# Optimization experiments

Hardware: AMD Instinct MI355X
Metric: run time of the kernel (lower is better)

## Reference

```python
import jax, jax.numpy as jnp
import numpy as np

N_NODES = 100000
N_EDGES = 1600000
N_FEAT = 128
HIDDEN = 128
N_CLASSES = 64


def setup_inputs() -> dict:
    key = jax.random.key(0)
    ks = jax.random.split(key, 6)
    x = jax.random.normal(ks[0], (N_NODES, N_FEAT), dtype=jnp.float32)
    edge_index = jax.random.randint(ks[1], (2, N_EDGES), 0, N_NODES, dtype=jnp.int64)
    # Glorot-ish scaled weights
    W1_l = jax.random.normal(ks[2], (N_FEAT, HIDDEN), dtype=jnp.float32) / np.sqrt(N_FEAT)
    W1_r = jax.random.normal(ks[3], (N_FEAT, HIDDEN), dtype=jnp.float32) / np.sqrt(N_FEAT)
    W2_l = jax.random.normal(ks[4], (HIDDEN, N_CLASSES), dtype=jnp.float32) / np.sqrt(HIDDEN)
    W2_r = jax.random.normal(ks[5], (HIDDEN, N_CLASSES), dtype=jnp.float32) / np.sqrt(HIDDEN)
    b1 = jnp.zeros((HIDDEN,), dtype=jnp.float32)
    b2 = jnp.zeros((N_CLASSES,), dtype=jnp.float32)
    return {"x": x, "edge_index": edge_index, "W1_l": W1_l, "b1": b1,
            "W1_r": W1_r, "W2_l": W2_l, "b2": b2, "W2_r": W2_r}


def _sage_conv(h, src, dst, n_nodes, inv_deg, W_l, W_r, b):
    # mean aggregation of source-node features into destination nodes
    agg = jax.ops.segment_sum(h[src], dst, num_segments=n_nodes)  # [N, d]
    agg = agg * inv_deg[:, None]
    return agg @ W_l + h @ W_r + b


def reference(x, edge_index, W1_l, b1, W1_r, W2_l, b2, W2_r):
    src, dst = edge_index[0], edge_index[1]
    n = x.shape[0]
    deg = jax.ops.segment_sum(jnp.ones_like(dst, dtype=x.dtype), dst, num_segments=n)
    inv_deg = 1.0 / jnp.maximum(deg, 1.0)
    h = jax.nn.relu(_sage_conv(x, src, dst, n, inv_deg, W1_l, W1_r, b1))
    # dropout is identity in eval mode
    out = _sage_conv(h, src, dst, n, inv_deg, W2_l, W2_r, b2)
    return out
```

## Files before the change

### kernel.cpp

```cpp
#include <hip/hip_runtime.h>

#define N_NODES   100000
#define N_EDGES   1600000
#define BSHIFT    9
#define NB        196

typedef __attribute__((ext_vector_type(8))) short short8;
typedef __attribute__((ext_vector_type(4))) float f32x4;
typedef __attribute__((ext_vector_type(2))) float f32x2;

__device__ __forceinline__ unsigned short f2bf(float f) {
    unsigned u = __float_as_uint(f);
    u += 0x7FFF + ((u >> 16) & 1);
    return (unsigned short)(u >> 16);
}
__device__ __forceinline__ float bf2f(short s) {
    return __uint_as_float(((unsigned)(unsigned short)s) << 16);
}

__device__ __forceinline__ int load_src(const int* e, int is64, int i) {
    return is64 ? e[2 * i] : e[i];
}
__device__ __forceinline__ int load_dst(const int* e, int is64, int i) {
    return is64 ? e[2 * (N_EDGES + i)] : e[N_EDGES + i];
}

__device__ __forceinline__ int block_detect_is64(const int* e, int* s_nz) {
    if (threadIdx.x == 0) *s_nz = 0;
    __syncthreads();
    int v = 0;
    for (int i = threadIdx.x; i < 1024; i += 256) v |= e[2 * i + 1];
    if (v) atomicOr(s_nz, 1);
    __syncthreads();
    return (*s_nz == 0) ? 1 : 0;
}

__global__ __launch_bounds__(256) void phaseA_kernel(
        const int* __restrict__ e, const float* __restrict__ x,
        const float* __restrict__ W1_l, const float* __restrict__ W1_r,
        const float* __restrict__ W2_l, const float* __restrict__ W2_r,
        int* __restrict__ bcnt, short* __restrict__ xb,
        unsigned int* __restrict__ xq,
        short* __restrict__ W1t, short* __restrict__ W2lt, short* __restrict__ W2rt) {
    const int blk = blockIdx.x;
    if (blk < 391) {
        __shared__ int s_nz;
        __shared__ int s_cnt[NB];
        for (int t = threadIdx.x; t < NB; t += 256) s_cnt[t] = 0;
        int is64 = block_detect_is64(e, &s_nz);
        __syncthreads();
        int i0 = blk * 4096;
        int n = min(4096, N_EDGES - i0);
        for (int t = 0; t < 16; t++) {
            int k = t * 256 + threadIdx.x;
            if (k < n) {
                int d = load_dst(e, is64, i0 + k);
                atomicAdd(&s_cnt[d >> BSHIFT], 1);
            }
        }
        __syncthreads();
        for (int t = threadIdx.x; t < NB; t += 256)
            if (s_cnt[t]) atomicAdd(&bcnt[t], s_cnt[t]);
    } else if (blk < 12891) {
        int t = (blk - 391) * 256 + threadIdx.x;
        int i = t * 4;
        float4 v = *(const float4*)&x[i];
        short4 o;
        o.x = (short)f2bf(v.x); o.y = (short)f2bf(v.y);
        o.z = (short)f2bf(v.z); o.w = (short)f2bf(v.w);
        *(short4*)&xb[i] = o;
        int w = __builtin_amdgcn_cvt_pk_fp8_f32(v.x, v.y, 0, false);
        w = __builtin_amdgcn_cvt_pk_fp8_f32(v.z, v.w, w, true);
        xq[t] = (unsigned int)w;
    } else {
        int i = (blk - 12891) * 256 + threadIdx.x;
        if (i < 32768) {
            int n = i >> 8, k = i & 255;
            float v = (k < 128) ? W1_l[k * 128 + n] : W1_r[(k - 128) * 128 + n];
            W1t[i] = (short)f2bf(v);
        } else if (i < 40960) {
            int j = i - 32768, n = j >> 7, k = j & 127;
            W2lt[j] = (short)f2bf(W2_l[k * 64 + n]);
        } else {
            int j = i - 40960, n = j >> 7, k = j & 127;
            W2rt[j] = (short)f2bf(W2_r[k * 64 + n]);
        }
    }
}

__global__ __launch_bounds__(256) void binscat_kernel(
        const int* __restrict__ e, const int* __restrict__ bcnt,
        int* __restrict__ boff, int2* __restrict__ pairs) {
    __shared__ int2 s_pairs[4096];
    __shared__ int s_cnt[256], s_off[256], s_base[256], s_cur[256];
    __shared__ int s_nz;
    const int tid = threadIdx.x;
    s_cnt[tid] = 0;
    int is64 = block_detect_is64(e, &s_nz);
    __syncthreads();
    int i0 = blockIdx.x * 4096;
    int n = min(4096, N_EDGES - i0);
    int ls[16], ld[16];
    #pragma unroll
    for (int t = 0; t < 16; t++) {
        int k = t * 256 + tid;
        if (k < n) {
            ls[t] = load_src(e, is64, i0 + k);
            ld[t] = load_dst(e, is64, i0 + k);
            atomicAdd(&s_cnt[ld[t] >> BSHIFT], 1);
        }
    }
    __syncthreads();
    int lv = s_cnt[tid];
    s_off[tid] = lv;
    __syncthreads();
    for (int off = 1; off < 256; off <<= 1) {
        int t = (tid >= off) ? s_off[tid - off] : 0;
        __syncthreads();
        s_off[tid] += t;
        __syncthreads();
    }
    int excl = s_off[tid] - lv;
    int gv = (tid < NB) ? bcnt[tid] : 0;
    s_base[tid] = gv;
    __syncthreads();
    for (int off = 1; off < 256; off <<= 1) {
        int t = (tid >= off) ? s_base[tid - off] : 0;
        __syncthreads();
        s_base[tid] += t;
        __syncthreads();
    }
    int bst = s_base[tid] - gv;
    int gb = 0;
    if (tid < NB && lv > 0) gb = atomicAdd(&boff[tid], lv);
    s_off[tid] = excl;
    s_base[tid] = bst + gb;
    s_cur[tid] = excl;
    __syncthreads();
    #pragma unroll
    for (int t = 0; t < 16; t++) {
        int k = t * 256 + tid;
        if (k < n) {
            int pos = atomicAdd(&s_cur[ld[t] >> BSHIFT], 1);
            s_pairs[pos] = (int2){ls[t], ld[t]};
        }
    }
    __syncthreads();
    for (int j = tid; j < n; j += 256) {
        int2 pr = s_pairs[j];
        int b = pr.y >> BSHIFT;
        pairs[s_base[b] + (j - s_off[b])] = pr;
    }
}

__global__ __launch_bounds__(256) void fused_fill_kernel(
        const int* __restrict__ bcnt, const int2* __restrict__ pairs,
        int* __restrict__ deg_i, int* __restrict__ cursor,
        float* __restrict__ inv_deg, int* __restrict__ col) {
    __shared__ int ldeg[512];
    __shared__ int ssum[256];
    __shared__ int sp0;
    const int tid = threadIdx.x;
    const int b = blockIdx.x;
    const int nbase = b << BSHIFT;
    int gv = (tid < NB) ? bcnt[tid] : 0;
    ssum[tid] = gv;
    __syncthreads();
    for (int off = 1; off < 256; off <<= 1) {
        int t = (tid >= off) ? ssum[tid - off] : 0;
        __syncthreads();
        ssum[tid] += t;
        __syncthreads();
    }
    if (tid == b) sp0 = ssum[tid] - gv;
    ldeg[tid] = 0; ldeg[tid + 256] = 0;
    __syncthreads();
    const int p0 = sp0, cnt = bcnt[b];
    for (int j = tid; j < cnt; j += 256)
        atomicAdd(&ldeg[pairs[p0 + j].y - nbase], 1);
    __syncthreads();
    int d0 = ldeg[tid * 2], d1 = ldeg[tid * 2 + 1];
    int tsum = d0 + d1;
    ssum[tid] = tsum;
    __syncthreads();
    for (int off = 1; off < 256; off <<= 1) {
        int t = (tid >= off) ? ssum[tid - off] : 0;
        __syncthreads();
        ssum[tid] += t;
        __syncthreads();
    }
    int excl = ssum[tid] - tsum;
    int s0 = p0 + excl;
    int s1 = s0 + d0;
    ldeg[tid * 2] = s0;
    ldeg[tid * 2 + 1] = s1;
    int idx0 = nbase + tid * 2;
    if (idx0 < N_NODES) {
        deg_i[idx0] = d0;
        cursor[idx0] = s0;
        inv_deg[idx0] = 1.0f / fmaxf((float)d0, 1.0f);
    }
    if (idx0 + 1 < N_NODES) {
        deg_i[idx0 + 1] = d1;
        cursor[idx0 + 1] = s1;
        inv_deg[idx0 + 1] = 1.0f / fmaxf((float)d1, 1.0f);
    }
    __syncthreads();
    for (int j = tid; j < cnt; j += 256) {
        int2 pr = pairs[p0 + j];
        int pos = atomicAdd(&ldeg[pr.y - nbase], 1);
        col[pos] = pr.x;
    }
}

__device__ __forceinline__ void acc_fp8x8(float* acc, uint2 w) {
    f32x2 f;
    f = __builtin_amdgcn_cvt_pk_f32_fp8((int)w.x, false); acc[0] += f[0]; acc[1] += f[1];
    f = __builtin_amdgcn_cvt_pk_f32_fp8((int)w.x, true);  acc[2] += f[0]; acc[3] += f[1];
    f = __builtin_amdgcn_cvt_pk_f32_fp8((int)w.y, false); acc[4] += f[0]; acc[5] += f[1];
    f = __builtin_amdgcn_cvt_pk_f32_fp8((int)w.y, true);  acc[6] += f[0]; acc[7] += f[1];
}

__global__ __launch_bounds__(256) void agg128_kernel(
        const int* __restrict__ cursor, const int* __restrict__ deg_i,
        const int* __restrict__ col, const unsigned int* __restrict__ xq,
        const float* __restrict__ inv_deg, short* __restrict__ agg) {
    int node = blockIdx.x * 16 + (threadIdx.x >> 4);
    int lane = threadIdx.x & 15;
    int cnt = deg_i[node];
    int start = cursor[node];
    float acc[8] = {0.f};
    int k = 0;
    for (; k + 4 <= cnt; k += 4) {
        int s0 = col[start + k + 0];
        int s1 = col[start + k + 1];
        int s2 = col[start + k + 2];
        int s3 = col[start + k + 3];
        uint2 w0 = *(const uint2*)(xq + (size_t)s0 * 32 + lane * 2);
        uint2 w1 = *(const uint2*)(xq + (size_t)s1 * 32 + lane * 2);
        uint2 w2 = *(const uint2*)(xq + (size_t)s2 * 32 + lane * 2);
        uint2 w3 = *(const uint2*)(xq + (size_t)s3 * 32 + lane * 2);
        acc_fp8x8(acc, w0); acc_fp8x8(acc, w1);
        acc_fp8x8(acc, w2); acc_fp8x8(acc, w3);
    }
    for (; k < cnt; k++) {
        int s0 = col[start + k];
        uint2 w = *(const uint2*)(xq + (size_t)s0 * 32 + lane * 2);
        acc_fp8x8(acc, w);
    }
    float sc = inv_deg[node];
    short8 o;
    #pragma unroll
    for (int j = 0; j < 8; j++) o[j] = (short)f2bf(acc[j] * sc);
    *(short8*)(agg + (size_t)node * 128 + lane * 8) = o;
}

__global__ __launch_bounds__(256) void agg64_kernel(
        const int* __restrict__ cursor, const int* __restrict__ deg_i,
        const int* __restrict__ col, const unsigned int* __restrict__ pq,
        const float* __restrict__ inv_deg, float* __restrict__ out) {
    int node = blockIdx.x * 32 + (threadIdx.x >> 3);
    int lane = threadIdx.x & 7;
    int cnt = deg_i[node];
    int start = cursor[node];
    float acc[8] = {0.f};
    int k = 0;
    for (; k + 4 <= cnt; k += 4) {
        int s0 = col[start + k + 0];
        int s1 = col[start + k + 1];
        int s2 = col[start + k + 2];
        int s3 = col[start + k + 3];
        uint2 w0 = *(const uint2*)(pq + (size_t)s0 * 16 + lane * 2);
        uint2 w1 = *(const uint2*)(pq + (size_t)s1 * 16 + lane * 2);
        uint2 w2 = *(const uint2*)(pq + (size_t)s2 * 16 + lane * 2);
        uint2 w3 = *(const uint2*)(pq + (size_t)s3 * 16 + lane * 2);
        acc_fp8x8(acc, w0); acc_fp8x8(acc, w1);
        acc_fp8x8(acc, w2); acc_fp8x8(acc, w3);
    }
    for (; k < cnt; k++) {
        int s0 = col[start + k];
        uint2 w = *(const uint2*)(pq + (size_t)s0 * 16 + lane * 2);
        acc_fp8x8(acc, w);
    }
    float sc = inv_deg[node];
    float* dst = out + (size_t)node * 64 + lane * 8;
    float4 o0 = *(float4*)dst;
    float4 o1 = *(float4*)(dst + 4);
    o0.x += acc[0] * sc; o0.y += acc[1] * sc; o0.z += acc[2] * sc; o0.w += acc[3] * sc;
    o1.x += acc[4] * sc; o1.y += acc[5] * sc; o1.z += acc[6] * sc; o1.w += acc[7] * sc;
    *(float4*)dst = o0;
    *(float4*)(dst + 4) = o1;
}

__global__ __launch_bounds__(256, 2) void gemm1_mfma(
        const short* __restrict__ agg1, const short* __restrict__ xb,
        const short* __restrict__ W1t, const float* __restrict__ b1,
        short* __restrict__ h) {
    const int wave = threadIdx.x >> 6, lane = threadIdx.x & 63;
    const int m = lane & 15, q = lane >> 4;
    const int wid = blockIdx.x * 4 + wave;
    const int half = wid & 1;
    short8 breg[4][8];
    #pragma unroll
    for (int t = 0; t < 4; t++)
        #pragma unroll
        for (int c = 0; c < 8; c++)
            breg[t][c] = *(const short8*)(W1t + (size_t)(half * 64 + t * 16 + m) * 256 + c * 32 + q * 8);
    float bias[4];
    #pragma unroll
    for (int t = 0; t < 4; t++) bias[t] = b1[half * 64 + t * 16 + m];

    for (int tile = wid >> 1; tile < 6250; tile += 1024) {
        const short* arow = agg1 + (size_t)(tile * 16 + m) * 128;
        const short* xrow = xb + (size_t)(tile * 16 + m) * 128;
        short8 a[8];
        #pragma unroll
        for (int c = 0; c < 4; c++) a[c] = *(const short8*)(arow + c * 32 + q * 8);
        #pragma unroll
        for (int c = 0; c < 4; c++) a[c + 4] = *(const short8*)(xrow + c * 32 + q * 8);
        f32x4 acc[4];
        #pragma unroll
        for (int t = 0; t < 4; t++) acc[t] = (f32x4){0.f, 0.f, 0.f, 0.f};
        #pragma unroll
        for (int c = 0; c < 8; c++)
            #pragma unroll
            for (int t = 0; t < 4; t++)
                acc[t] = __builtin_amdgcn_mfma_f32_16x16x32_bf16(a[c], breg[t][c], acc[t], 0, 0, 0);
        #pragma unroll
        for (int t = 0; t < 4; t++) {
            int colc = half * 64 + t * 16 + m;
            #pragma unroll
            for (int r = 0; r < 4; r++) {
                int rr = tile * 16 + q * 4 + r;
                h[(size_t)rr * 128 + colc] = (short)f2bf(fmaxf(acc[t][r] + bias[t], 0.f));
            }
        }
    }
}

__global__ __launch_bounds__(256, 2) void proj2_mfma(
        const short* __restrict__ h, const short* __restrict__ W2lt,
        const short* __restrict__ W2rt, const float* __restrict__ b2,
        unsigned char* __restrict__ p8, float* __restrict__ out) {
    const int wave = threadIdx.x >> 6, lane = threadIdx.x & 63;
    const int m = lane & 15, q = lane >> 4;
    const int wid = blockIdx.x * 4 + wave;
    short8 bl[4][4], br[4][4];
    #pragma unroll
    for (int t = 0; t < 4; t++)
        #pragma unroll
        for (int c = 0; c < 4; c++) {
            bl[t][c] = *(const short8*)(W2lt + (size_t)(t * 16 + m) * 128 + c * 32 + q * 8);
            br[t][c] = *(const short8*)(W2rt + (size_t)(t * 16 + m) * 128 + c * 32 + q * 8);
        }
    float bias[4];
    #pragma unroll
    for (int t = 0; t < 4; t++) bias[t] = b2[t * 16 + m];

    for (int tile = wid; tile < 6250; tile += 2048) {
        const short* hrow = h + (size_t)(tile * 16 + m) * 128;
        short8 a[4];
        #pragma unroll
        for (int c = 0; c < 4; c++) a[c] = *(const short8*)(hrow + c * 32 + q * 8);
        f32x4 accp[4], acco[4];
        #pragma unroll
        for (int t = 0; t < 4; t++) {
            accp[t] = (f32x4){0.f, 0.f, 0.f, 0.f};
            acco[t] = (f32x4){0.f, 0.f, 0.f, 0.f};
        }
        #pragma unroll
        for (int c = 0; c < 4; c++)
            #pragma unroll
            for (int t = 0; t < 4; t++) {
                accp[t] = __builtin_amdgcn_mfma_f32_16x16x32_bf16(a[c], bl[t][c], accp[t], 0, 0, 0);
                acco[t] = __builtin_amdgcn_mfma_f32_16x16x32_bf16(a[c], br[t][c], acco[t], 0, 0, 0);
            }
        #pragma unroll
        for (int t = 0; t < 4; t++) {
            int colc = t * 16 + m;
            #pragma unroll
            for (int r = 0; r < 4; r++) {
                int rr = tile * 16 + q * 4 + r;
                float pv = accp[t][r];
                int w = __builtin_amdgcn_cvt_pk_fp8_f32(pv, pv, 0, false);
                p8[(size_t)rr * 64 + colc] = (unsigned char)(w & 0xFF);
                out[(size_t)rr * 64 + colc] = acco[t][r] + bias[t];
            }
        }
    }
}

extern "C" void kernel_launch(void* const* d_in, const int* in_sizes, int n_in,
                              void* d_out, int out_size, void* d_ws, size_t ws_size,
                              hipStream_t stream) {
    const float* x    = (const float*)d_in[0];
    const int*   edge = (const int*)d_in[1];
    const float* W1_l = (const float*)d_in[2];
    const float* b1   = (const float*)d_in[3];
    const float* W1_r = (const float*)d_in[4];
    const float* W2_l = (const float*)d_in[5];
    const float* b2   = (const float*)d_in[6];
    const float* W2_r = (const float*)d_in[7];
    float* out = (float*)d_out;

    int* iw = (int*)d_ws;
    int* deg_i  = iw;
    int* cursor = iw + 100000;
    int* col    = iw + 200000;
    int* bcnt   = iw + 1800000;
    int* boff   = iw + 1800256;
    float* inv_deg = (float*)iw + 1800832;
    int2*  pairs   = (int2*)(iw + 1900928);
    short* xb   = (short*)(iw + 5100928);
    short* hb   = xb + 12800000;
    short* ag1  = hb + 12800000;
    short* W1t  = ag1 + 12800000;
    short* W2lt = W1t + 32768;
    short* W2rt = W2lt + 8192;
    unsigned int* xq = (unsigned int*)hb;
    unsigned char* p8 = (unsigned char*)ag1;
    unsigned int*  pq = (unsigned int*)ag1;

    hipMemsetAsync(bcnt, 0, 512 * sizeof(int), stream);

    phaseA_kernel<<<13083, 256, 0, stream>>>(edge, x, W1_l, W1_r, W2_l, W2_r,
                                             bcnt, xb, xq, W1t, W2lt, W2rt);
    binscat_kernel<<<391, 256, 0, stream>>>(edge, bcnt, boff, pairs);
    fused_fill_kernel<<<NB, 256, 0, stream>>>(bcnt, pairs, deg_i, cursor, inv_deg, col);

    agg128_kernel<<<6250, 256, 0, stream>>>(cursor, deg_i, col, xq, inv_deg, ag1);
    gemm1_mfma<<<512, 256, 0, stream>>>(ag1, xb, W1t, b1, hb);

    proj2_mfma<<<512, 256, 0, stream>>>(hb, W2lt, W2rt, b2, p8, out);
    agg64_kernel<<<3125, 256, 0, stream>>>(cursor, deg_i, col, pq, inv_deg, out);
}
```

Baseline: 268.5 us.

## Fuse layer-1 neighbor aggregation with MFMA GEMM via shared-memory tile

The separate fp8 gather-aggregation kernel and the layer-1 bf16 MFMA GEMM are merged into one persistent kernel. Each block aggregates 16 nodes into an LDS tile and then runs the GEMM on that tile, so the aggregated features never make a round trip through global memory. The fp8 copy of x is moved to the ag1 buffer so it no longer aliases the h output. In exchange, each wave now holds only a 32-column weight slice, there are two block barriers per tile, and the gather and MFMA phases are serialized within a block, which may lower latency hiding.

```diff
diff --git a/kernel.cpp b/kernel.cpp
--- a/kernel.cpp
+++ b/kernel.cpp
@@ -13,9 +13,6 @@
     unsigned u = __float_as_uint(f);
     u += 0x7FFF + ((u >> 16) & 1);
     return (unsigned short)(u >> 16);
-}
-__device__ __forceinline__ float bf2f(short s) {
-    return __uint_as_float(((unsigned)(unsigned short)s) << 16);
 }
 
 __device__ __forceinline__ int load_src(const int* e, int is64, int i) {
@@ -221,38 +218,88 @@
     f = __builtin_amdgcn_cvt_pk_f32_fp8((int)w.y, true);  acc[6] += f[0]; acc[7] += f[1];
 }
 
-__global__ __launch_bounds__(256) void agg128_kernel(
+#define AGS 136
+__global__ __launch_bounds__(256, 3) void layer1_fused(
         const int* __restrict__ cursor, const int* __restrict__ deg_i,
         const int* __restrict__ col, const unsigned int* __restrict__ xq,
-        const float* __restrict__ inv_deg, short* __restrict__ agg) {
-    int node = blockIdx.x * 16 + (threadIdx.x >> 4);
-    int lane = threadIdx.x & 15;
-    int cnt = deg_i[node];
-    int start = cursor[node];
-    float acc[8] = {0.f};
-    int k = 0;
-    for (; k + 4 <= cnt; k += 4) {
-        int s0 = col[start + k + 0];
-        int s1 = col[start + k + 1];
-        int s2 = col[start + k + 2];
-        int s3 = col[start + k + 3];
-        uint2 w0 = *(const uint2*)(xq + (size_t)s0 * 32 + lane * 2);
-        uint2 w1 = *(const uint2*)(xq + (size_t)s1 * 32 + lane * 2);
-        uint2 w2 = *(const uint2*)(xq + (size_t)s2 * 32 + lane * 2);
-        uint2 w3 = *(const uint2*)(xq + (size_t)s3 * 32 + lane * 2);
-        acc_fp8x8(acc, w0); acc_fp8x8(acc, w1);
-        acc_fp8x8(acc, w2); acc_fp8x8(acc, w3);
-    }
-    for (; k < cnt; k++) {
-        int s0 = col[start + k];
-        uint2 w = *(const uint2*)(xq + (size_t)s0 * 32 + lane * 2);
-        acc_fp8x8(acc, w);
-    }
-    float sc = inv_deg[node];
-    short8 o;
-    #pragma unroll
-    for (int j = 0; j < 8; j++) o[j] = (short)f2bf(acc[j] * sc);
-    *(short8*)(agg + (size_t)node * 128 + lane * 8) = o;
+        const float* __restrict__ inv_deg, const short* __restrict__ xb,
+        const short* __restrict__ W1t, const float* __restrict__ b1,
+        short* __restrict__ h) {
+    __shared__ short s_ag[16 * AGS];
+    const int wave = threadIdx.x >> 6, lane = threadIdx.x & 63;
+    const int m = lane & 15, q = lane >> 4;
+    short8 breg[2][8];
+    #pragma unroll
+    for (int t = 0; t < 2; t++)
+        #pragma unroll
+        for (int c = 0; c < 8; c++)
+            breg[t][c] = *(const short8*)(W1t + (size_t)(wave * 32 + t * 16 + m) * 256 + c * 32 + q * 8);
+    float bias[2];
+    #pragma unroll
+    for (int t = 0; t < 2; t++) bias[t] = b1[wave * 32 + t * 16 + m];
+
+    const int n16 = threadIdx.x >> 4;
+    const int l16 = threadIdx.x & 15;
+
+    for (int tile = blockIdx.x; tile < 6250; tile += gridDim.x) {
+        {
+            int node = tile * 16 + n16;
+            int cnt = deg_i[node];
+            int start = cursor[node];
+            float acc[8] = {0.f};
+            int k = 0;
+            for (; k + 4 <= cnt; k += 4) {
+                int s0 = col[start + k + 0];
+                int s1 = col[start + k + 1];
+                int s2 = col[start + k + 2];
+                int s3 = col[start + k + 3];
+                uint2 w0 = *(const uint2*)(xq + (size_t)s0 * 32 + l16 * 2);
+                uint2 w1 = *(const uint2*)(xq + (size_t)s1 * 32 + l16 * 2);
+                uint2 w2 = *(const uint2*)(xq + (size_t)s2 * 32 + l16 * 2);
+                uint2 w3 = *(const uint2*)(xq + (size_t)s3 * 32 + l16 * 2);
+                acc_fp8x8(acc, w0); acc_fp8x8(acc, w1);
+                acc_fp8x8(acc, w2); acc_fp8x8(acc, w3);
+            }
+            for (; k < cnt; k++) {
+                int s0 = col[start + k];
+                uint2 w = *(const uint2*)(xq + (size_t)s0 * 32 + l16 * 2);
+                acc_fp8x8(acc, w);
+            }
+            float sc = inv_deg[node];
+            short8 o;
+            #pragma unroll
+            for (int j = 0; j < 8; j++) o[j] = (short)f2bf(acc[j] * sc);
+            *(short8*)&s_ag[n16 * AGS + l16 * 8] = o;
+        }
+        __syncthreads();
+        {
+            const short* xrow = xb + (size_t)(tile * 16 + m) * 128;
+            short8 a[8];
+            #pragma unroll
+            for (int c = 0; c < 4; c++) a[c] = *(const short8*)&s_ag[m * AGS + c * 32 + q * 8];
+            #pragma unroll
+            for (int c = 0; c < 4; c++) a[c + 4] = *(const short8*)(xrow + c * 32 + q * 8);
+            f32x4 acc2[2];
+            #pragma unroll
+            for (int t = 0; t < 2; t++) acc2[t] = (f32x4){0.f, 0.f, 0.f, 0.f};
+            #pragma unroll
+            for (int c = 0; c < 8; c++)
+                #pragma unroll
+                for (int t = 0; t < 2; t++)
+                    acc2[t] = __builtin_amdgcn_mfma_f32_16x16x32_bf16(a[c], breg[t][c], acc2[t], 0, 0, 0);
+            #pragma unroll
+            for (int t = 0; t < 2; t++) {
+                int colc = wave * 32 + t * 16 + m;
+                float bs = bias[t];
+                #pragma unroll
+                for (int r = 0; r < 4; r++) {
+                    int rr = tile * 16 + q * 4 + r;
+                    h[(size_t)rr * 128 + colc] = (short)f2bf(fmaxf(acc2[t][r] + bs, 0.f));
+                }
+            }
+        }
+        __syncthreads();
+    }
 }
 
 __global__ __launch_bounds__(256) void agg64_kernel(
@@ -292,52 +339,6 @@
     *(float4*)(dst + 4) = o1;
 }
 
-__global__ __launch_bounds__(256, 2) void gemm1_mfma(
-        const short* __restrict__ agg1, const short* __restrict__ xb,
-        const short* __restrict__ W1t, const float* __restrict__ b1,
-        short* __restrict__ h) {
-    const int wave = threadIdx.x >> 6, lane = threadIdx.x & 63;
-    const int m = lane & 15, q = lane >> 4;
-    const int wid = blockIdx.x * 4 + wave;
-    const int half = wid & 1;
-    short8 breg[4][8];
-    #pragma unroll
-    for (int t = 0; t < 4; t++)
-        #pragma unroll
-        for (int c = 0; c < 8; c++)
-            breg[t][c] = *(const short8*)(W1t + (size_t)(half * 64 + t * 16 + m) * 256 + c * 32 + q * 8);
-    float bias[4];
-    #pragma unroll
-    for (int t = 0; t < 4; t++) bias[t] = b1[half * 64 + t * 16 + m];
-
-    for (int tile = wid >> 1; tile < 6250; tile += 1024) {
-        const short* arow = agg1 + (size_t)(tile * 16 + m) * 128;
-        const short* xrow = xb + (size_t)(tile * 16 + m) * 128;
-        short8 a[8];
-        #pragma unroll
-        for (int c = 0; c < 4; c++) a[c] = *(const short8*)(arow + c * 32 + q * 8);
-        #pragma unroll
-        for (int c = 0; c < 4; c++) a[c + 4] = *(const short8*)(xrow + c * 32 + q * 8);
-        f32x4 acc[4];
-        #pragma unroll
-        for (int t = 0; t < 4; t++) acc[t] = (f32x4){0.f, 0.f, 0.f, 0.f};
-        #pragma unroll
-        for (int c = 0; c < 8; c++)
-            #pragma unroll
-            for (int t = 0; t < 4; t++)
-                acc[t] = __builtin_amdgcn_mfma_f32_16x16x32_bf16(a[c], breg[t][c], acc[t], 0, 0, 0);
-        #pragma unroll
-        for (int t = 0; t < 4; t++) {
-            int colc = half * 64 + t * 16 + m;
-            #pragma unroll
-            for (int r = 0; r < 4; r++) {
-                int rr = tile * 16 + q * 4 + r;
-                h[(size_t)rr * 128 + colc] = (short)f2bf(fmaxf(acc[t][r] + bias[t], 0.f));
-            }
-        }
-    }
-}
-
 __global__ __launch_bounds__(256, 2) void proj2_mfma(
         const short* __restrict__ h, const short* __restrict__ W2lt,
         const short* __restrict__ W2rt, const float* __restrict__ b2,
@@ -418,6 +419,7 @@
     short* W2lt = W1t + 32768;
     short* W2rt = W2lt + 8192;
     unsigned int* xq = (unsigned int*)hb;
+    xq = (unsigned int*)ag1;
     unsigned char* p8 = (unsigned char*)ag1;
     unsigned int*  pq = (unsigned int*)ag1;
 
@@ -428,8 +430,8 @@
     binscat_kernel<<<391, 256, 0, stream>>>(edge, bcnt, boff, pairs);
     fused_fill_kernel<<<NB, 256, 0, stream>>>(bcnt, pairs, deg_i, cursor, inv_deg, col);
 
-    agg128_kernel<<<6250, 256, 0, stream>>>(cursor, deg_i, col, xq, inv_deg, ag1);
-    gemm1_mfma<<<512, 256, 0, stream>>>(ag1, xb, W1t, b1, hb);
+    layer1_fused<<<1024, 256, 0, stream>>>(cursor, deg_i, col, xq, inv_deg,
+                                           xb, W1t, b1, hb);
 
     proj2_mfma<<<512, 256, 0, stream>>>(hb, W2lt, W2rt, b2, p8, out);
     agg64_kernel<<<3125, 256, 0, stream>>>(cursor, deg_i, col, pq, inv_deg, out);
```

Measured after the change: 273.3 us. No clear change (+1.8%).
